# Kernel tuning notes

Hardware: AMD Instinct MI355X
Metric: run time of the kernel (lower is better)

The kernel has to match this reference:

```python
import jax, jax.numpy as jnp
import numpy as np

B, N, DIM = 4, 4096, 1024
HEADS, DIM_HEAD, BSZ, EPS = 8, 64, 16, 1e-8
INNER = HEADS * DIM_HEAD


def setup_inputs() -> dict:
    key = jax.random.key(0)
    k1, k2, k3 = jax.random.split(key, 3)
    x = jax.random.normal(k1, (B, N, DIM), dtype=jnp.float32)
    # torch nn.Linear weights are [out, in]; scale ~ fan_in^-0.5 for stable exp()
    w_qkv = jax.random.normal(k2, (3 * INNER, DIM), dtype=jnp.float32) * (DIM ** -0.5)
    w_out = jax.random.normal(k3, (DIM, INNER), dtype=jnp.float32) * (INNER ** -0.5)
    b_out = jnp.zeros((DIM,), dtype=jnp.float32)
    return {"x": x, "w_qkv": w_qkv, "w_out": w_out, "b_out": b_out}


def _to_bh(t, b, n):
    # 'b n (h d) -> (b h) n d'
    return t.reshape(b, n, HEADS, DIM_HEAD).transpose(0, 2, 1, 3).reshape(b * HEADS, n, DIM_HEAD)


def _to_blocks(t):
    # 'b (n z) d -> b n z d'
    return t.reshape(t.shape[0], -1, BSZ, DIM_HEAD)


def _calc_Y_and_A(qb, kb, vb):
    S = jnp.einsum('bnid,bnjd->bnij', qb, kb)   # block-local scores
    A = jnp.exp(S)
    y = jnp.einsum('bnij,bnjd->bnid', A, vb)
    return y.reshape(y.shape[0], -1, DIM_HEAD), A.sum(-1).reshape(A.shape[0], -1)


def _hattention(x, w_qkv, w_out, b_out):
    b, n, _ = x.shape
    qkv = x @ w_qkv.T
    q, k, v = jnp.split(qkv, 3, axis=-1)
    q, k, v = (_to_bh(t, b, n) for t in (q, k, v))
    q = q * (DIM_HEAD ** -0.5)

    num_levels = int(np.log2(n // BSZ)) - 1
    qkvs = [(q, k, v)]
    for _ in range(num_levels):
        q = q.reshape(q.shape[0], -1, 2, DIM_HEAD).mean(axis=2)
        k = k.reshape(k.shape[0], -1, 2, DIM_HEAD).mean(axis=2)
        v = v.reshape(v.shape[0], -1, 2, DIM_HEAD).sum(axis=2)
        qkvs.append((q, k, v))
    top_level = qkvs[0]
    coarse_levels = qkvs[1:][::-1]  # coarsest first

    Ys = []
    for (ql, kl, vl) in coarse_levels:
        qb, kb, vb = map(_to_blocks, (ql, kl, vl))
        bh, nb = kb.shape[0], kb.shape[1]
        # flip sibling key blocks: 'b (n r) z d' with r=2 reversed
        kb = kb.reshape(bh, nb // 2, 2, BSZ, DIM_HEAD)[:, :, ::-1].reshape(bh, nb, BSZ, DIM_HEAD)
        Ys.append(_calc_Y_and_A(qb, kb, vb))
    Ys.append(_calc_Y_and_A(*map(_to_blocks, top_level)))

    Y, A = Ys[0]
    for y_l, a_l in Ys[1:]:
        Y = jnp.repeat(Y, 2, axis=1) + y_l
        A = jnp.repeat(A, 2, axis=1) + a_l

    out = Y / (A + EPS)[..., None]
    # '(b h) n d -> b n (h d)'
    out = out.reshape(b, HEADS, n, DIM_HEAD).transpose(0, 2, 1, 3).reshape(b, n, INNER)
    return out @ w_out.T + b_out


def reference(x, w_qkv, w_out, b_out):
    return _hattention(x, w_qkv, w_out, b_out)
```

## Files before the change

### kernel.cpp

```cpp
#include <hip/hip_runtime.h>
#include <hip/hip_bf16.h>
#include <cstdio>


typedef __bf16 bf16x8 __attribute__((ext_vector_type(8)));
typedef float floatx4 __attribute__((ext_vector_type(4)));
typedef unsigned short ushortx8 __attribute__((ext_vector_type(8)));
typedef unsigned int uintx4 __attribute__((ext_vector_type(4)));

#define ROWS_PER_BH 8160

__device__ __forceinline__ void g2lds16(const void* g, void* l) {
  __builtin_amdgcn_global_load_lds(
      (const __attribute__((address_space(1))) void*)g,
      (__attribute__((address_space(3))) void*)l, 16, 0, 0);
}

__device__ __forceinline__ unsigned short f2bu(float x) {
  __hip_bfloat16 h = __float2bfloat16(x);
  return *(unsigned short*)&h;
}
__device__ __forceinline__ float bu2f(unsigned short u) {
  __hip_bfloat16 h = *(__hip_bfloat16*)&u;
  return __bfloat162float(h);
}

__global__ __launch_bounds__(256) void f2b_kernel(const float* __restrict__ s,
                                                  __hip_bfloat16* __restrict__ d,
                                                  int n) {
  int i0 = (blockIdx.x * 256 + threadIdx.x) * 4;
  if (i0 + 3 < n) {
    float4 v = *(const float4*)(s + i0);
    d[i0 + 0] = __float2bfloat16(v.x);
    d[i0 + 1] = __float2bfloat16(v.y);
    d[i0 + 2] = __float2bfloat16(v.z);
    d[i0 + 3] = __float2bfloat16(v.w);
  }
}

__global__ __launch_bounds__(256) void gemm_qkv_kernel(
    const unsigned short* __restrict__ A,
    const unsigned short* __restrict__ B,
    __hip_bfloat16* __restrict__ qp, __hip_bfloat16* __restrict__ kp,
    __hip_bfloat16* __restrict__ vp) {
  const int K = 1024;
  __shared__ unsigned short ldsA[128 * 32];
  __shared__ unsigned short ldsB[128 * 32];
  const int tid = threadIdx.x;
  const int lane = tid & 63, w = tid >> 6;
  const int wm = w >> 1, wn = w & 1;
  const int tM = blockIdx.x * 128, tN = blockIdx.y * 128;

  const unsigned short* Ag = A + (size_t)(tM + w * 32 + (lane >> 2)) * K + (lane & 3) * 8;
  const unsigned short* Bg = B + (size_t)(tN + w * 32 + (lane >> 2)) * K + (lane & 3) * 8;
  unsigned short* lA = &ldsA[w * 1024 + lane * 8];
  unsigned short* lB = &ldsB[w * 1024 + lane * 8];

  floatx4 acc[4][4];
#pragma unroll
  for (int i = 0; i < 4; i++)
#pragma unroll
    for (int j = 0; j < 4; j++) acc[i][j] = (floatx4){0.f, 0.f, 0.f, 0.f};

  const int rA = wm * 64 + (lane & 15);
  const int rB = wn * 64 + (lane & 15);
  const int kc = (lane >> 4) * 8;

  for (int kt = 0; kt < K; kt += 32) {
    __syncthreads();
    g2lds16(Ag + kt, lA);
    g2lds16(Ag + 16 * K + kt, lA + 512);
    g2lds16(Bg + kt, lB);
    g2lds16(Bg + 16 * K + kt, lB + 512);
    __syncthreads();
    bf16x8 af[4], bv[4];
#pragma unroll
    for (int i = 0; i < 4; i++) af[i] = *(const bf16x8*)&ldsA[(rA + i * 16) * 32 + kc];
#pragma unroll
    for (int j = 0; j < 4; j++) bv[j] = *(const bf16x8*)&ldsB[(rB + j * 16) * 32 + kc];
#pragma unroll
    for (int i = 0; i < 4; i++)
#pragma unroll
      for (int j = 0; j < 4; j++)
        acc[i][j] = __builtin_amdgcn_mfma_f32_16x16x32_bf16(af[i], bv[j], acc[i][j], 0, 0, 0);
  }

  const int quad = lane >> 4;
#pragma unroll
  for (int i = 0; i < 4; i++) {
#pragma unroll
    for (int j = 0; j < 4; j++) {
      const int c = tN + wn * 64 + j * 16 + (lane & 15);
      const int tensor = c >> 9;
      const int rem = c & 511;
      const int h = rem >> 6, d = rem & 63;
      __hip_bfloat16* dstbuf = (tensor == 0) ? qp : ((tensor == 1) ? kp : vp);
      const float scale = (tensor == 0) ? 0.125f : 1.0f;
#pragma unroll
      for (int r = 0; r < 4; r++) {
        const int m = tM + wm * 64 + i * 16 + quad * 4 + r;
        const int b = m >> 12, n = m & 4095;
        size_t dst = ((size_t)(b * 8 + h) * ROWS_PER_BH + n) * 64 + d;
        dstbuf[dst] = __float2bfloat16(acc[i][j][r] * scale);
      }
    }
  }
}

__global__ __launch_bounds__(256) void gemm_out_kernel(
    const unsigned short* __restrict__ A,
    const unsigned short* __restrict__ B,
    const float* __restrict__ bias, float* __restrict__ out) {
  const int K = 512;
  __shared__ unsigned short ldsA[128 * 32];
  __shared__ unsigned short ldsB[128 * 32];
  const int tid = threadIdx.x;
  const int lane = tid & 63, w = tid >> 6;
  const int wm = w >> 1, wn = w & 1;
  const int tM = blockIdx.x * 128, tN = blockIdx.y * 128;

  const unsigned short* Ag = A + (size_t)(tM + w * 32 + (lane >> 2)) * K + (lane & 3) * 8;
  const unsigned short* Bg = B + (size_t)(tN + w * 32 + (lane >> 2)) * K + (lane & 3) * 8;
  unsigned short* lA = &ldsA[w * 1024 + lane * 8];
  unsigned short* lB = &ldsB[w * 1024 + lane * 8];

  floatx4 acc[4][4];
#pragma unroll
  for (int i = 0; i < 4; i++)
#pragma unroll
    for (int j = 0; j < 4; j++) acc[i][j] = (floatx4){0.f, 0.f, 0.f, 0.f};

  const int rA = wm * 64 + (lane & 15);
  const int rB = wn * 64 + (lane & 15);
  const int kc = (lane >> 4) * 8;

  for (int kt = 0; kt < K; kt += 32) {
    __syncthreads();
    g2lds16(Ag + kt, lA);
    g2lds16(Ag + 16 * K + kt, lA + 512);
    g2lds16(Bg + kt, lB);
    g2lds16(Bg + 16 * K + kt, lB + 512);
    __syncthreads();
    bf16x8 af[4], bv[4];
#pragma unroll
    for (int i = 0; i < 4; i++) af[i] = *(const bf16x8*)&ldsA[(rA + i * 16) * 32 + kc];
#pragma unroll
    for (int j = 0; j < 4; j++) bv[j] = *(const bf16x8*)&ldsB[(rB + j * 16) * 32 + kc];
#pragma unroll
    for (int i = 0; i < 4; i++)
#pragma unroll
      for (int j = 0; j < 4; j++)
        acc[i][j] = __builtin_amdgcn_mfma_f32_16x16x32_bf16(af[i], bv[j], acc[i][j], 0, 0, 0);
  }

  const int quad = lane >> 4;
#pragma unroll
  for (int i = 0; i < 4; i++) {
#pragma unroll
    for (int j = 0; j < 4; j++) {
      const int c = tN + wn * 64 + j * 16 + (lane & 15);
      const float bb = bias[c];
#pragma unroll
      for (int r = 0; r < 4; r++) {
        const int m = tM + wm * 64 + i * 16 + quad * 4 + r;
        out[(size_t)m * 1024 + c] = acc[i][j][r] + bb;
      }
    }
  }
}

__global__ __launch_bounds__(256) void pyramid_kernel(
    __hip_bfloat16* __restrict__ qp, __hip_bfloat16* __restrict__ kp,
    __hip_bfloat16* __restrict__ vp, int srcRow, int dstRow, int nOut, int shift) {
  int idx = blockIdx.x * 256 + threadIdx.x;
  if (idx >= 32 * nOut * 64) return;
  int d = idx & 63;
  int i = (idx >> 6) & (nOut - 1);
  int bh = idx >> (6 + shift);
  size_t s0 = ((size_t)bh * ROWS_PER_BH + srcRow + 2 * i) * 64 + d;
  size_t dst = ((size_t)bh * ROWS_PER_BH + dstRow + i) * 64 + d;
  float q0 = __bfloat162float(qp[s0]), q1 = __bfloat162float(qp[s0 + 64]);
  float k0 = __bfloat162float(kp[s0]), k1 = __bfloat162float(kp[s0 + 64]);
  float v0 = __bfloat162float(vp[s0]), v1 = __bfloat162float(vp[s0 + 64]);
  qp[dst] = __float2bfloat16(0.5f * (q0 + q1));
  kp[dst] = __float2bfloat16(0.5f * (k0 + k1));
  vp[dst] = __float2bfloat16(v0 + v1);
}

__global__ __launch_bounds__(256) void attn_kernel(
    const unsigned short* __restrict__ qp, const unsigned short* __restrict__ kp,
    const unsigned short* __restrict__ vp, float* __restrict__ yall,
    float* __restrict__ aall) {
  __shared__ __align__(16) unsigned short vT[4][64 * 24];
  const int w = threadIdx.x >> 6, lane = threadIdx.x & 63;
  const int g = blockIdx.x * 4 + w;
  if (g >= 510) return;
  const int bh = blockIdx.y;
  int level, blk;
  if (g < 256)      { level = 0; blk = g; }
  else if (g < 384) { level = 1; blk = g - 256; }
  else if (g < 448) { level = 2; blk = g - 384; }
  else if (g < 480) { level = 3; blk = g - 448; }
  else if (g < 496) { level = 4; blk = g - 480; }
  else if (g < 504) { level = 5; blk = g - 496; }
  else if (g < 508) { level = 6; blk = g - 504; }
  else              { level = 7; blk = g - 508; }
  const int ro = 8192 - (8192 >> level);
  const int kblk = (level == 0) ? blk : (blk ^ 1);
  const int m = lane & 15, q = lane >> 4;
  const size_t qbase = ((size_t)bh * ROWS_PER_BH + ro + blk * 16) * 64;
  const size_t kbase = ((size_t)bh * ROWS_PER_BH + ro + kblk * 16) * 64;

  const bf16x8 ka0 = *(const bf16x8*)(kp + kbase + m * 64 + q * 8);
  const bf16x8 ka1 = *(const bf16x8*)(kp + kbase + m * 64 + 32 + q * 8);
  const bf16x8 qb0 = *(const bf16x8*)(qp + qbase + m * 64 + q * 8);
  const bf16x8 qb1 = *(const bf16x8*)(qp + qbase + m * 64 + 32 + q * 8);

  const ushortx8 v0 = *(const ushortx8*)(vp + qbase + m * 64 + q * 16);
  const ushortx8 v1 = *(const ushortx8*)(vp + qbase + m * 64 + q * 16 + 8);
  unsigned short* vtw = vT[w];
#pragma unroll
  for (int j = 0; j < 8; j++) vtw[(q * 16 + j) * 24 + m] = v0[j];
#pragma unroll
  for (int j = 0; j < 8; j++) vtw[(q * 16 + 8 + j) * 24 + m] = v1[j];

  floatx4 s = (floatx4){0.f, 0.f, 0.f, 0.f};
  s = __builtin_amdgcn_mfma_f32_16x16x32_bf16(ka0, qb0, s, 0, 0, 0);
  s = __builtin_amdgcn_mfma_f32_16x16x32_bf16(ka1, qb1, s, 0, 0, 0);

  unsigned short pb0 = f2bu(__expf(s[0])), pb1 = f2bu(__expf(s[1]));
  unsigned short pb2 = f2bu(__expf(s[2])), pb3 = f2bu(__expf(s[3]));
  float asum = bu2f(pb0) + bu2f(pb1) + bu2f(pb2) + bu2f(pb3);
  asum += __shfl_xor(asum, 16, 64);
  asum += __shfl_xor(asum, 32, 64);
  const size_t arow = (size_t)bh * ROWS_PER_BH + ro + blk * 16;
  if (q == 0) aall[arow + m] = asum;

  unsigned int d0 = (unsigned int)pb0 | ((unsigned int)pb1 << 16);
  unsigned int d1 = (unsigned int)pb2 | ((unsigned int)pb3 << 16);
  const int s0l = m + 32 * (q & 1);
  unsigned int u0 = __shfl(d0, s0l, 64);
  unsigned int u1 = __shfl(d1, s0l, 64);
  unsigned int u2 = __shfl(d0, s0l + 16, 64);
  unsigned int u3 = __shfl(d1, s0l + 16, 64);
  union { uintx4 i; bf16x8 b; } pau;
  pau.i = (q < 2) ? (uintx4){u0, u1, u2, u3} : (uintx4){0u, 0u, 0u, 0u};
  const bf16x8 pa = pau.b;

  const bf16x8 bz = pau.b;
#pragma unroll
  for (int c = 0; c < 4; c++) {
    union { uintx4 i; bf16x8 b; } bvu;
    bvu.i = (uintx4){0u, 0u, 0u, 0u};
    if (q < 2) bvu.b = *(const bf16x8*)&vtw[(c * 16 + m) * 24 + q * 8];
    floatx4 y = (floatx4){0.f, 0.f, 0.f, 0.f};
    y = __builtin_amdgcn_mfma_f32_16x16x32_bf16(pa, bvu.b, y, 0, 0, 0);
#pragma unroll
    for (int r = 0; r < 4; r++)
      yall[(arow + q * 4 + r) * 64 + c * 16 + m] = y[r];
  }
  (void)bz;
}

__global__ __launch_bounds__(256) void combine_kernel(
    const float* __restrict__ yall, const float* __restrict__ aall,
    __hip_bfloat16* __restrict__ Ub) {
  int idx = blockIdx.x * 256 + threadIdx.x;
  int d = idx & 63;
  int i = (idx >> 6) & 4095;
  int bh = idx >> 18;
  size_t base = (size_t)bh * ROWS_PER_BH;
  float Y = 0.f, Aa = 0.f;
#pragma unroll
  for (int l = 0; l < 8; l++) {
    int r = (8192 - (8192 >> l)) + (i >> l);
    Y += yall[(base + r) * 64 + d];
    Aa += aall[base + r];
  }
  float u = Y / (Aa + 1e-8f);
  int b = bh >> 3, h = bh & 7;
  size_t m = (size_t)b * 4096 + i;
  Ub[m * 512 + (size_t)h * 64 + d] = __float2bfloat16(u);
}

extern "C" void kernel_launch(void* const* d_in, const int* in_sizes, int n_in,
                              void* d_out, int out_size, void* d_ws, size_t ws_size,
                              hipStream_t stream) {
  const float* x     = (const float*)d_in[0];
  const float* w_qkv = (const float*)d_in[1];
  const float* w_out = (const float*)d_in[2];
  const float* b_out = (const float*)d_in[3];
  float* out = (float*)d_out;

  char* ws = (char*)d_ws;
  __hip_bfloat16* xb    = (__hip_bfloat16*)(ws + 0);
  __hip_bfloat16* wqkvb = (__hip_bfloat16*)(ws + 33554432);
  __hip_bfloat16* wob   = (__hip_bfloat16*)(ws + 36700160);
  __hip_bfloat16* qp    = (__hip_bfloat16*)(ws + 37748736);
  __hip_bfloat16* kp    = (__hip_bfloat16*)(ws + 71172096);
  __hip_bfloat16* vp    = (__hip_bfloat16*)(ws + 104595456);
  float* yall           = (float*)(ws + 138018816);
  float* aall           = (float*)(ws + 204865536);
  __hip_bfloat16* Ub    = (__hip_bfloat16*)(ws + 205910016);
  if (ws_size < 222687232ULL)
    fprintf(stderr, "HAttention1D: ws too small: %zu < 222687232\n", ws_size);

  f2b_kernel<<<16384, 256, 0, stream>>>(x, xb, 16777216);
  f2b_kernel<<<1536, 256, 0, stream>>>(w_qkv, wqkvb, 1572864);
  f2b_kernel<<<512, 256, 0, stream>>>(w_out, wob, 524288);

  gemm_qkv_kernel<<<dim3(128, 12), 256, 0, stream>>>(
      (const unsigned short*)xb, (const unsigned short*)wqkvb, qp, kp, vp);

  const int offs[8] = {0, 4096, 6144, 7168, 7680, 7936, 8064, 8128};
  const int nls[8]  = {4096, 2048, 1024, 512, 256, 128, 64, 32};
  for (int l = 1; l <= 7; ++l) {
    int nOut = nls[l];
    int shift = 0; while ((1 << shift) < nOut) shift++;
    pyramid_kernel<<<nOut * 8, 256, 0, stream>>>(qp, kp, vp, offs[l - 1], offs[l], nOut, shift);
  }

  attn_kernel<<<dim3(128, 32), 256, 0, stream>>>(
      (const unsigned short*)qp, (const unsigned short*)kp,
      (const unsigned short*)vp, yall, aall);

  combine_kernel<<<32768, 256, 0, stream>>>(yall, aall, Ub);

  gemm_out_kernel<<<dim3(128, 8), 256, 0, stream>>>(
      (const unsigned short*)Ub, (const unsigned short*)wob, b_out, out);
}
```

Measured before the change: 307.5 us.

## Fuse pyramid levels into one kernel, deepen GEMM K-tile with swizzle, store Y in bf16

The seven per-level pyramid launches become a single kernel. Each block loads 128 rows of q/k/v into shared memory and builds every coarser level in place, which removes repeated global reads and launch overhead. The shared GEMM core now loads 64-wide K tiles with an XOR-swizzled LDS layout, halving the barrier count and reducing bank conflicts. The per-level attention outputs are stored as bf16 instead of fp32, halving traffic into the combine kernel at some cost in precision.

```diff
diff --git a/kernel.cpp b/kernel.cpp
--- a/kernel.cpp
+++ b/kernel.cpp
@@ -1,6 +1,5 @@
 #include <hip/hip_runtime.h>
 #include <hip/hip_bf16.h>
-#include <cstdio>
 
 
 typedef __bf16 bf16x8 __attribute__((ext_vector_type(8)));
@@ -38,52 +37,70 @@
   }
 }
 
+template <int K>
+__device__ __forceinline__ void gemm_core(const unsigned short* __restrict__ A,
+                                          const unsigned short* __restrict__ B,
+                                          unsigned short* ldsA, unsigned short* ldsB,
+                                          int tM, int tN, floatx4 acc[4][4]) {
+  const int tid = threadIdx.x;
+  const int lane = tid & 63, w = tid >> 6;
+  const int wm = w >> 1, wn = w & 1;
+  const int lr = lane >> 3;
+  const int gch = (lane & 7) ^ lr;
+  const unsigned short* Ag = A + (size_t)(tM + w * 32 + lr) * K + gch * 8;
+  const unsigned short* Bg = B + (size_t)(tN + w * 32 + lr) * K + gch * 8;
+  unsigned short* lA = &ldsA[w * 2048 + lane * 8];
+  unsigned short* lB = &ldsB[w * 2048 + lane * 8];
+
+  const int rA = wm * 64 + (lane & 15);
+  const int rB = wn * 64 + (lane & 15);
+  const int quad = lane >> 4;
+  const int sw = lane & 7;
+
+  for (int kt = 0; kt < K; kt += 64) {
+    __syncthreads();
+#pragma unroll
+    for (int c = 0; c < 4; c++) {
+      g2lds16(Ag + (size_t)(c * 8) * K + kt, lA + c * 512);
+      g2lds16(Bg + (size_t)(c * 8) * K + kt, lB + c * 512);
+    }
+    __syncthreads();
+#pragma unroll
+    for (int kk = 0; kk < 2; kk++) {
+      bf16x8 af[4], bv[4];
+#pragma unroll
+      for (int i = 0; i < 4; i++)
+        af[i] = *(const bf16x8*)&ldsA[(rA + i * 16) * 64 + (((kk * 4 + quad) ^ sw) * 8)];
+#pragma unroll
+      for (int j = 0; j < 4; j++)
+        bv[j] = *(const bf16x8*)&ldsB[(rB + j * 16) * 64 + (((kk * 4 + quad) ^ sw) * 8)];
+#pragma unroll
+      for (int i = 0; i < 4; i++)
+#pragma unroll
+        for (int j = 0; j < 4; j++)
+          acc[i][j] = __builtin_amdgcn_mfma_f32_16x16x32_bf16(af[i], bv[j], acc[i][j], 0, 0, 0);
+    }
+  }
+}
+
 __global__ __launch_bounds__(256) void gemm_qkv_kernel(
     const unsigned short* __restrict__ A,
     const unsigned short* __restrict__ B,
     __hip_bfloat16* __restrict__ qp, __hip_bfloat16* __restrict__ kp,
     __hip_bfloat16* __restrict__ vp) {
-  const int K = 1024;
-  __shared__ unsigned short ldsA[128 * 32];
-  __shared__ unsigned short ldsB[128 * 32];
-  const int tid = threadIdx.x;
-  const int lane = tid & 63, w = tid >> 6;
+  __shared__ unsigned short ldsA[128 * 64];
+  __shared__ unsigned short ldsB[128 * 64];
+  const int lane = threadIdx.x & 63, w = threadIdx.x >> 6;
   const int wm = w >> 1, wn = w & 1;
   const int tM = blockIdx.x * 128, tN = blockIdx.y * 128;
 
-  const unsigned short* Ag = A + (size_t)(tM + w * 32 + (lane >> 2)) * K + (lane & 3) * 8;
-  const unsigned short* Bg = B + (size_t)(tN + w * 32 + (lane >> 2)) * K + (lane & 3) * 8;
-  unsigned short* lA = &ldsA[w * 1024 + lane * 8];
-  unsigned short* lB = &ldsB[w * 1024 + lane * 8];
-
   floatx4 acc[4][4];
 #pragma unroll
   for (int i = 0; i < 4; i++)
 #pragma unroll
     for (int j = 0; j < 4; j++) acc[i][j] = (floatx4){0.f, 0.f, 0.f, 0.f};
 
-  const int rA = wm * 64 + (lane & 15);
-  const int rB = wn * 64 + (lane & 15);
-  const int kc = (lane >> 4) * 8;
-
-  for (int kt = 0; kt < K; kt += 32) {
-    __syncthreads();
-    g2lds16(Ag + kt, lA);
-    g2lds16(Ag + 16 * K + kt, lA + 512);
-    g2lds16(Bg + kt, lB);
-    g2lds16(Bg + 16 * K + kt, lB + 512);
-    __syncthreads();
-    bf16x8 af[4], bv[4];
-#pragma unroll
-    for (int i = 0; i < 4; i++) af[i] = *(const bf16x8*)&ldsA[(rA + i * 16) * 32 + kc];
-#pragma unroll
-    for (int j = 0; j < 4; j++) bv[j] = *(const bf16x8*)&ldsB[(rB + j * 16) * 32 + kc];
-#pragma unroll
-    for (int i = 0; i < 4; i++)
-#pragma unroll
-      for (int j = 0; j < 4; j++)
-        acc[i][j] = __builtin_amdgcn_mfma_f32_16x16x32_bf16(af[i], bv[j], acc[i][j], 0, 0, 0);
-  }
+  gemm_core<1024>(A, B, ldsA, ldsB, tM, tN, acc);
 
   const int quad = lane >> 4;
 #pragma unroll
@@ -111,47 +128,19 @@
     const unsigned short* __restrict__ A,
     const unsigned short* __restrict__ B,
     const float* __restrict__ bias, float* __restrict__ out) {
-  const int K = 512;
-  __shared__ unsigned short ldsA[128 * 32];
-  __shared__ unsigned short ldsB[128 * 32];
-  const int tid = threadIdx.x;
-  const int lane = tid & 63, w = tid >> 6;
+  __shared__ unsigned short ldsA[128 * 64];
+  __shared__ unsigned short ldsB[128 * 64];
+  const int lane = threadIdx.x & 63, w = threadIdx.x >> 6;
   const int wm = w >> 1, wn = w & 1;
   const int tM = blockIdx.x * 128, tN = blockIdx.y * 128;
 
-  const unsigned short* Ag = A + (size_t)(tM + w * 32 + (lane >> 2)) * K + (lane & 3) * 8;
-  const unsigned short* Bg = B + (size_t)(tN + w * 32 + (lane >> 2)) * K + (lane & 3) * 8;
-  unsigned short* lA = &ldsA[w * 1024 + lane * 8];
-  unsigned short* lB = &ldsB[w * 1024 + lane * 8];
-
   floatx4 acc[4][4];
 #pragma unroll
   for (int i = 0; i < 4; i++)
 #pragma unroll
     for (int j = 0; j < 4; j++) acc[i][j] = (floatx4){0.f, 0.f, 0.f, 0.f};
 
-  const int rA = wm * 64 + (lane & 15);
-  const int rB = wn * 64 + (lane & 15);
-  const int kc = (lane >> 4) * 8;
-
-  for (int kt = 0; kt < K; kt += 32) {
-    __syncthreads();
-    g2lds16(Ag + kt, lA);
-    g2lds16(Ag + 16 * K + kt, lA + 512);
-    g2lds16(Bg + kt, lB);
-    g2lds16(Bg + 16 * K + kt, lB + 512);
-    __syncthreads();
-    bf16x8 af[4], bv[4];
-#pragma unroll
-    for (int i = 0; i < 4; i++) af[i] = *(const bf16x8*)&ldsA[(rA + i * 16) * 32 + kc];
-#pragma unroll
-    for (int j = 0; j < 4; j++) bv[j] = *(const bf16x8*)&ldsB[(rB + j * 16) * 32 + kc];
-#pragma unroll
-    for (int i = 0; i < 4; i++)
-#pragma unroll
-      for (int j = 0; j < 4; j++)
-        acc[i][j] = __builtin_amdgcn_mfma_f32_16x16x32_bf16(af[i], bv[j], acc[i][j], 0, 0, 0);
-  }
+  gemm_core<512>(A, B, ldsA, ldsB, tM, tN, acc);
 
   const int quad = lane >> 4;
 #pragma unroll
@@ -169,27 +158,54 @@
   }
 }
 
-__global__ __launch_bounds__(256) void pyramid_kernel(
+__global__ __launch_bounds__(256) void pyramid_all_kernel(
     __hip_bfloat16* __restrict__ qp, __hip_bfloat16* __restrict__ kp,
-    __hip_bfloat16* __restrict__ vp, int srcRow, int dstRow, int nOut, int shift) {
-  int idx = blockIdx.x * 256 + threadIdx.x;
-  if (idx >= 32 * nOut * 64) return;
-  int d = idx & 63;
-  int i = (idx >> 6) & (nOut - 1);
-  int bh = idx >> (6 + shift);
-  size_t s0 = ((size_t)bh * ROWS_PER_BH + srcRow + 2 * i) * 64 + d;
-  size_t dst = ((size_t)bh * ROWS_PER_BH + dstRow + i) * 64 + d;
-  float q0 = __bfloat162float(qp[s0]), q1 = __bfloat162float(qp[s0 + 64]);
-  float k0 = __bfloat162float(kp[s0]), k1 = __bfloat162float(kp[s0 + 64]);
-  float v0 = __bfloat162float(vp[s0]), v1 = __bfloat162float(vp[s0 + 64]);
-  qp[dst] = __float2bfloat16(0.5f * (q0 + q1));
-  kp[dst] = __float2bfloat16(0.5f * (k0 + k1));
-  vp[dst] = __float2bfloat16(v0 + v1);
+    __hip_bfloat16* __restrict__ vp) {
+  __shared__ unsigned short qs[128 * 64], ks[128 * 64], vs[128 * 64];
+  const int bh = blockIdx.x >> 5;
+  const int chunk = blockIdx.x & 31;
+  const int tid = threadIdx.x;
+  const size_t base = (size_t)bh * ROWS_PER_BH;
+  const size_t g0 = (base + chunk * 128) * 64;
+  const unsigned short* qg = (const unsigned short*)qp;
+  const unsigned short* kg = (const unsigned short*)kp;
+  const unsigned short* vg = (const unsigned short*)vp;
+#pragma unroll
+  for (int c = 0; c < 4; c++) {
+    int off = c * 2048 + tid * 8;
+    *(ushortx8*)&qs[off] = *(const ushortx8*)(qg + g0 + off);
+    *(ushortx8*)&ks[off] = *(const ushortx8*)(kg + g0 + off);
+    *(ushortx8*)&vs[off] = *(const ushortx8*)(vg + g0 + off);
+  }
+  const int offs[8] = {0, 4096, 6144, 7168, 7680, 7936, 8064, 8128};
+#pragma unroll
+  for (int l = 1; l <= 7; l++) {
+    __syncthreads();
+    const int nOut = 128 >> l;
+    for (int e = tid; e < nOut * 32; e += 256) {
+      const int i = e >> 5, dp = (e & 31) * 2;
+      const int a = (i << l) * 64 + dp;
+      const int b = a + (1 << (l - 1)) * 64;
+      unsigned short q0 = f2bu(0.5f * (bu2f(qs[a]) + bu2f(qs[b])));
+      unsigned short q1 = f2bu(0.5f * (bu2f(qs[a + 1]) + bu2f(qs[b + 1])));
+      unsigned short k0 = f2bu(0.5f * (bu2f(ks[a]) + bu2f(ks[b])));
+      unsigned short k1 = f2bu(0.5f * (bu2f(ks[a + 1]) + bu2f(ks[b + 1])));
+      unsigned short v0 = f2bu(bu2f(vs[a]) + bu2f(vs[b]));
+      unsigned short v1 = f2bu(bu2f(vs[a + 1]) + bu2f(vs[b + 1]));
+      qs[a] = q0; qs[a + 1] = q1;
+      ks[a] = k0; ks[a + 1] = k1;
+      vs[a] = v0; vs[a + 1] = v1;
+      const size_t grow = (base + offs[l] + (size_t)chunk * nOut + i) * 64 + dp;
+      *(unsigned int*)((unsigned short*)qp + grow) = (unsigned int)q0 | ((unsigned int)q1 << 16);
+      *(unsigned int*)((unsigned short*)kp + grow) = (unsigned int)k0 | ((unsigned int)k1 << 16);
+      *(unsigned int*)((unsigned short*)vp + grow) = (unsigned int)v0 | ((unsigned int)v1 << 16);
+    }
+  }
 }
 
 __global__ __launch_bounds__(256) void attn_kernel(
     const unsigned short* __restrict__ qp, const unsigned short* __restrict__ kp,
-    const unsigned short* __restrict__ vp, float* __restrict__ yall,
+    const unsigned short* __restrict__ vp, __hip_bfloat16* __restrict__ yall,
     float* __restrict__ aall) {
   __shared__ __align__(16) unsigned short vT[4][64 * 24];
   const int w = threadIdx.x >> 6, lane = threadIdx.x & 63;
@@ -247,7 +263,6 @@
   pau.i = (q < 2) ? (uintx4){u0, u1, u2, u3} : (uintx4){0u, 0u, 0u, 0u};
   const bf16x8 pa = pau.b;
 
-  const bf16x8 bz = pau.b;
 #pragma unroll
   for (int c = 0; c < 4; c++) {
     union { uintx4 i; bf16x8 b; } bvu;
@@ -257,13 +272,12 @@
     y = __builtin_amdgcn_mfma_f32_16x16x32_bf16(pa, bvu.b, y, 0, 0, 0);
 #pragma unroll
     for (int r = 0; r < 4; r++)
-      yall[(arow + q * 4 + r) * 64 + c * 16 + m] = y[r];
-  }
-  (void)bz;
+      yall[(arow + q * 4 + r) * 64 + c * 16 + m] = __float2bfloat16(y[r]);
+  }
 }
 
 __global__ __launch_bounds__(256) void combine_kernel(
-    const float* __restrict__ yall, const float* __restrict__ aall,
+    const unsigned short* __restrict__ yall, const float* __restrict__ aall,
     __hip_bfloat16* __restrict__ Ub) {
   int idx = blockIdx.x * 256 + threadIdx.x;
   int d = idx & 63;
@@ -274,7 +288,7 @@
 #pragma unroll
   for (int l = 0; l < 8; l++) {
     int r = (8192 - (8192 >> l)) + (i >> l);
-    Y += yall[(base + r) * 64 + d];
+    Y += bu2f(yall[(base + r) * 64 + d]);
     Aa += aall[base + r];
   }
   float u = Y / (Aa + 1e-8f);
@@ -299,11 +313,9 @@
   __hip_bfloat16* qp    = (__hip_bfloat16*)(ws + 37748736);
   __hip_bfloat16* kp    = (__hip_bfloat16*)(ws + 71172096);
   __hip_bfloat16* vp    = (__hip_bfloat16*)(ws + 104595456);
-  float* yall           = (float*)(ws + 138018816);
-  float* aall           = (float*)(ws + 204865536);
-  __hip_bfloat16* Ub    = (__hip_bfloat16*)(ws + 205910016);
-  if (ws_size < 222687232ULL)
-    fprintf(stderr, "HAttention1D: ws too small: %zu < 222687232\n", ws_size);
+  __hip_bfloat16* yall  = (__hip_bfloat16*)(ws + 138018816);
+  float* aall           = (float*)(ws + 171442176);
+  __hip_bfloat16* Ub    = (__hip_bfloat16*)(ws + 172486656);
 
   f2b_kernel<<<16384, 256, 0, stream>>>(x, xb, 16777216);
   f2b_kernel<<<1536, 256, 0, stream>>>(w_qkv, wqkvb, 1572864);
@@ -312,19 +324,13 @@
   gemm_qkv_kernel<<<dim3(128, 12), 256, 0, stream>>>(
       (const unsigned short*)xb, (const unsigned short*)wqkvb, qp, kp, vp);
 
-  const int offs[8] = {0, 4096, 6144, 7168, 7680, 7936, 8064, 8128};
-  const int nls[8]  = {4096, 2048, 1024, 512, 256, 128, 64, 32};
-  for (int l = 1; l <= 7; ++l) {
-    int nOut = nls[l];
-    int shift = 0; while ((1 << shift) < nOut) shift++;
-    pyramid_kernel<<<nOut * 8, 256, 0, stream>>>(qp, kp, vp, offs[l - 1], offs[l], nOut, shift);
-  }
+  pyramid_all_kernel<<<1024, 256, 0, stream>>>(qp, kp, vp);
 
   attn_kernel<<<dim3(128, 32), 256, 0, stream>>>(
       (const unsigned short*)qp, (const unsigned short*)kp,
       (const unsigned short*)vp, yall, aall);
 
-  combine_kernel<<<32768, 256, 0, stream>>>(yall, aall, Ub);
+  combine_kernel<<<32768, 256, 0, stream>>>((const unsigned short*)yall, aall, Ub);
 
   gemm_out_kernel<<<dim3(128, 8), 256, 0, stream>>>(
       (const unsigned short*)Ub, (const unsigned short*)wob, b_out, out);
```

Result: faster. 276.1 us (-10.2%).
